# Performance work log

Hardware: AMD Instinct MI355X
Metric: run time of the kernel (lower is better)

The kernel has to match this reference:

```python
import jax, jax.numpy as jnp
import numpy as np

# dims per module source / chosen globals
B, LB = 4, 28            # new frames, buffered frames; M = B+LB = L = 32
DK, DV = 256, 32         # Dk=256 hardcoded; Dv = 4*len_of_lookup+4 with len_of_lookup=7
HS, WS = 64, 64          # H//8, W//8 with H=W=512
LMAX = 32                # memory cap L
TRAIN_SZ = 1000          # log base train_sz
ALPHA = 0.5              # blend coefficient (original inits 0, which zeroes the branch)
# log(L*h*w + h*w, train_sz) / sqrt(Dk)
SCALE = float(np.log(LMAX * HS * WS + HS * WS) / np.log(TRAIN_SZ) / np.sqrt(DK))


def _xavier(key, fan_in, fan_out):
    lim = np.sqrt(6.0 / (fan_in + fan_out))
    return jax.random.uniform(key, (fan_in, fan_out), jnp.float32, -lim, lim)


def setup_inputs() -> dict:
    key = jax.random.key(0)
    ks = jax.random.split(key, 7)
    return {
        "fc": jax.random.normal(ks[0], (B, DK, HS, WS), jnp.float32),
        "fm": jax.random.normal(ks[1], (B, DV, HS, WS), jnp.float32),
        "key_buffer": jax.random.normal(ks[2], (LB, DK, HS, WS), jnp.float32),
        "value_buffer": jax.random.normal(ks[3], (LB, DV, HS, WS), jnp.float32),
        "Q": _xavier(ks[4], DK, DK),
        "K": _xavier(ks[5], DK, DK),
        "V": _xavier(ks[6], DV, DV),
    }


def reference(fc, fm, key_buffer, value_buffer, Q, K, V):
    # matmul = einsum('ijkl,jm->imkl'): per-pixel channel mixing
    q = jnp.einsum('bdhw,de->behw', fc, Q)                      # [B,Dk,h,w]
    k = jnp.concatenate([jnp.einsum('bdhw,de->behw', fc, K), key_buffer], axis=0)    # [M,Dk,h,w]
    v = jnp.concatenate([jnp.einsum('bdhw,de->behw', fm, V), value_buffer], axis=0)  # [M,Dv,h,w]
    # current_batch (=1) < L, so no slicing of k/v on this step
    scores = SCALE * jnp.einsum('bdhw,mdhw->bmhw', q, k)        # [B,M,h,w]
    attn = jax.nn.softmax(scores, axis=-1)                      # NOTE: softmax over width axis, as in source (dim=-1)
    ctx = jnp.einsum('bmhw,mdhw->bdhw', attn, v)                # [B,Dv,h,w]
    return fm + ALPHA * ctx
```

## Files before the change

### kernel.cpp

```cpp
#include <hip/hip_runtime.h>
#include <hip/hip_bf16.h>
#include <cmath>

#define NB 4
#define NM 32
#define DKc 256
#define DVc 32
#define NP 4096

using bf16x8 = __attribute__((ext_vector_type(8))) short;
using f32x4  = __attribute__((ext_vector_type(4))) float;

__device__ __forceinline__ unsigned short f2bf(float f) {
    union { float f; unsigned u; } x; x.f = f;
    unsigned r = 0x7FFFu + ((x.u >> 16) & 1u);
    return (unsigned short)((x.u + r) >> 16);
}

__global__ __launch_bounds__(256) void k_prep(
    const float* __restrict__ fc, unsigned short* __restrict__ fcT,
    const float* __restrict__ Q, unsigned short* __restrict__ WTq,
    const float* __restrict__ K, unsigned short* __restrict__ WTk,
    const float* __restrict__ fm, const float* __restrict__ V, float* __restrict__ vproj) {
    int x = blockIdx.x;
    int t = threadIdx.x;
    if (x < 1056) {
        __shared__ float tile[64][65];
        const float* s; unsigned short* d; int R, C, r0, c0;
        if (x < 1024) {
            int bb = x >> 8, rest = x & 255;
            R = 256; C = 4096;
            r0 = (rest >> 6) * 64; c0 = (rest & 63) * 64;
            s = fc + (long)bb * 256 * 4096; d = fcT + (long)bb * 256 * 4096;
        } else {
            int i = x - 1024;
            int mat = i >> 4, idx = i & 15;
            R = 256; C = 256;
            r0 = (idx >> 2) * 64; c0 = (idx & 3) * 64;
            s = mat ? K : Q; d = mat ? WTk : WTq;
        }
        #pragma unroll
        for (int j = 0; j < 16; ++j) {
            int i = t + 256 * j;
            int r = i >> 6, c = i & 63;
            tile[r][c] = s[(long)(r0 + r) * C + c0 + c];
        }
        __syncthreads();
        #pragma unroll
        for (int j = 0; j < 8; ++j) {
            int i = t + 256 * j;
            int row = i >> 5;
            int pr = i & 31;
            float f0 = tile[2 * pr][row];
            float f1 = tile[2 * pr + 1][row];
            unsigned pack = (unsigned)f2bf(f0) | ((unsigned)f2bf(f1) << 16);
            reinterpret_cast<unsigned*>(d)[(((long)(c0 + row) * R + r0) >> 1) + pr] = pack;
        }
    } else {
        __shared__ float Vl[32][32];
        __shared__ float fml[32][256];
        int i = x - 1056;
        int b = i >> 4, p0 = (i & 15) * 256;
        #pragma unroll
        for (int j = 0; j < 4; ++j) { int ii = t + 256 * j; Vl[ii >> 5][ii & 31] = V[ii]; }
        for (int j = 0; j < 32; ++j) {
            int ii = t + 256 * j;
            int dd = ii >> 8, c = ii & 255;
            fml[dd][c] = fm[((long)b * DVc + dd) * NP + p0 + c];
        }
        __syncthreads();
        float acc[32];
        #pragma unroll
        for (int e = 0; e < 32; ++e) acc[e] = 0.f;
        for (int dd = 0; dd < 32; ++dd) {
            float fv = fml[dd][t];
            #pragma unroll
            for (int e = 0; e < 32; ++e) acc[e] += fv * Vl[dd][e];
        }
        #pragma unroll
        for (int e = 0; e < 32; ++e) vproj[((long)b * DVc + e) * NP + p0 + t] = acc[e];
    }
}

__global__ __launch_bounds__(256) void k_proj(
    const unsigned short* __restrict__ WTq, const unsigned short* __restrict__ WTk,
    const unsigned short* __restrict__ fcT,
    float* __restrict__ qproj, float* __restrict__ kproj) {
    int t = threadIdx.x;
    int wave = t >> 6, lane = t & 63;
    int y = blockIdx.y;
    int b = y & 3, mat = y >> 2;
    int p0 = blockIdx.x * 64;
    int ln = lane & 15, quad = lane >> 4;
    const unsigned short* WT = mat ? WTk : WTq;
    float* dst = mat ? kproj : qproj;
    int e0w = wave * 64;
    const unsigned short* bbase = fcT + ((long)b * NP + p0 + ln) * DKc + quad * 8;
    f32x4 acc[4][4] = {};
    for (int kk = 0; kk < DKc; kk += 32) {
        bf16x8 a[4], bb[4];
        #pragma unroll
        for (int i = 0; i < 4; ++i)
            a[i] = *reinterpret_cast<const bf16x8*>(WT + (long)(e0w + i * 16 + ln) * DKc + quad * 8 + kk);
        #pragma unroll
        for (int j = 0; j < 4; ++j)
            bb[j] = *reinterpret_cast<const bf16x8*>(bbase + (long)j * 16 * DKc + kk);
        #pragma unroll
        for (int i = 0; i < 4; ++i)
            #pragma unroll
            for (int j = 0; j < 4; ++j)
                acc[i][j] = __builtin_amdgcn_mfma_f32_16x16x32_bf16(a[i], bb[j], acc[i][j], 0, 0, 0);
    }
    #pragma unroll
    for (int i = 0; i < 4; ++i)
        #pragma unroll
        for (int j = 0; j < 4; ++j)
            #pragma unroll
            for (int r = 0; r < 4; ++r) {
                int e = e0w + i * 16 + quad * 4 + r, p = p0 + j * 16 + ln;
                dst[((long)b * DKc + e) * NP + p] = acc[i][j][r];
            }
}

__global__ __launch_bounds__(1024, 4) void k_fused(
    const float* __restrict__ qproj, const float* __restrict__ kproj,
    const float* __restrict__ kbuf, const float* __restrict__ vproj,
    const float* __restrict__ vbuf, const float* __restrict__ fm,
    float* __restrict__ out, float scale) {
    __shared__ float red[16 * 1099];
    __shared__ float sc[32][68];
    int t = threadIdx.x;
    int b = blockIdx.x >> 6, hrow = blockIdx.x & 63;
    int p0h = hrow * 64;
    int wave = t >> 6, lane = t & 63;
    int wq = lane & 15, egw = lane >> 4;
    int e0 = wave * 16 + egw * 4;
    int w0 = wq * 4;

    f32x4 qv[4];
    const float* qp = qproj + ((long)b * DKc + e0) * NP + p0h + w0;
    #pragma unroll
    for (int j = 0; j < 4; ++j) qv[j] = *reinterpret_cast<const f32x4*>(qp + (long)j * NP);

    #pragma unroll
    for (int mc = 0; mc < 2; ++mc) {
        f32x4 acc[16];
        #pragma unroll
        for (int mi = 0; mi < 16; ++mi) acc[mi] = (f32x4){0.f, 0.f, 0.f, 0.f};
        #pragma unroll
        for (int mi = 0; mi < 16; ++mi) {
            int m = mc * 16 + mi;
            const float* kp = (m < 4 ? kproj + (long)m * DKc * NP : kbuf + (long)(m - 4) * DKc * NP)
                              + (long)e0 * NP + p0h + w0;
            #pragma unroll
            for (int j = 0; j < 4; ++j) {
                f32x4 kv = *reinterpret_cast<const f32x4*>(kp + (long)j * NP);
                acc[mi] += qv[j] * kv;
            }
        }
        #pragma unroll
        for (int mi = 0; mi < 16; ++mi)
            #pragma unroll
            for (int c = 0; c < 4; ++c) {
                float v = acc[mi][c];
                v += __shfl_xor(v, 16);
                v += __shfl_xor(v, 32);
                acc[mi][c] = v;
            }
        if (lane < 16) {
            #pragma unroll
            for (int mi = 0; mi < 16; ++mi)
                *reinterpret_cast<f32x4*>(&red[wave * 1099 + mi * 69 + lane * 4]) = acc[mi];
        }
        __syncthreads();
        {
            int mr = t >> 6, w = t & 63;
            float s = 0.f;
            #pragma unroll
            for (int v = 0; v < 16; ++v) s += red[v * 1099 + mr * 69 + w];
            sc[mc * 16 + mr][w] = s * scale;
        }
        __syncthreads();
    }
    #pragma unroll
    for (int r = 0; r < 2; ++r) {
        int m = wave * 2 + r;
        float x = sc[m][lane];
        float mx = x;
        #pragma unroll
        for (int d = 1; d < 64; d <<= 1) mx = fmaxf(mx, __shfl_xor(mx, d));
        float e = __expf(x - mx);
        float sum = e;
        #pragma unroll
        for (int d = 1; d < 64; d <<= 1) sum += __shfl_xor(sum, d);
        sc[m][lane] = e / sum;
    }
    __syncthreads();
    {
        int dg = t >> 6, w = t & 63;
        float c0 = 0.f, c1 = 0.f;
        #pragma unroll
        for (int m = 0; m < NM; ++m) {
            float a = sc[m][w];
            const float* vp = (m < 4 ? vproj + (long)m * DVc * NP : vbuf + (long)(m - 4) * DVc * NP)
                              + (long)(dg * 2) * NP + p0h + w;
            c0 += a * vp[0];
            c1 += a * vp[NP];
        }
        long gi0 = ((long)b * DVc + dg * 2) * NP + p0h + w;
        long gi1 = gi0 + NP;
        out[gi0] = fm[gi0] + 0.5f * c0;
        out[gi1] = fm[gi1] + 0.5f * c1;
    }
}

extern "C" void kernel_launch(void* const* d_in, const int* in_sizes, int n_in,
                              void* d_out, int out_size, void* d_ws, size_t ws_size,
                              hipStream_t stream) {
    const float* fc = (const float*)d_in[0];
    const float* fm = (const float*)d_in[1];
    const float* kb = (const float*)d_in[2];
    const float* vb = (const float*)d_in[3];
    const float* Q  = (const float*)d_in[4];
    const float* K  = (const float*)d_in[5];
    const float* V  = (const float*)d_in[6];
    float* out = (float*)d_out;
    char* ws = (char*)d_ws;
    unsigned short* fcT   = (unsigned short*)(ws);
    unsigned short* WTq   = (unsigned short*)(ws + 8388608);
    unsigned short* WTk   = (unsigned short*)(ws + 8519680);
    float*          qproj = (float*)(ws + 8650752);
    float*          kproj = (float*)(ws + 25427968);
    float*          vproj = (float*)(ws + 42205184);
    float scale = (float)(log(135168.0) / log(1000.0) / 16.0);

    hipLaunchKernelGGL(k_prep, dim3(1120), dim3(256), 0, stream,
                       fc, fcT, Q, WTq, K, WTk, fm, V, vproj);
    hipLaunchKernelGGL(k_proj, dim3(64, 8), dim3(256), 0, stream,
                       WTq, WTk, fcT, qproj, kproj);
    hipLaunchKernelGGL(k_fused, dim3(256), dim3(1024), 0, stream,
                       qproj, kproj, kb, vproj, vb, fm, out, scale);
}
```

Measured before the change: 263.0 us.

## Split fused attention into score-partial kernel and softmax/output kernel

Replaces the single 1024-thread fused kernel with two kernels. k_scores computes partial q·k dot products over 32-channel chunks, using a grid spread over width segments, channel chunks and batch, with one pixel per thread and no LDS reduction. k_out sums the 8 partials, applies softmax and the value mix. The goal is more parallelism and simpler coalesced loads in the heavy key-read stage. The cost is an extra launch and a partial buffer round-trip through memory, and the partial buffer aliases the workspace region used by fcT.

```diff
diff --git a/kernel.cpp b/kernel.cpp
--- a/kernel.cpp
+++ b/kernel.cpp
@@ -122,69 +122,60 @@
             }
 }
 
-__global__ __launch_bounds__(1024, 4) void k_fused(
+__global__ __launch_bounds__(256, 2) void k_scores(
     const float* __restrict__ qproj, const float* __restrict__ kproj,
-    const float* __restrict__ kbuf, const float* __restrict__ vproj,
+    const float* __restrict__ kbuf, float* __restrict__ partial) {
+    int t = threadIdx.x;
+    int wseg = blockIdx.x, ec = blockIdx.y, b = blockIdx.z;
+    int w = wseg * 256 + t;
+    int e0 = ec * 32;
+    const float* qp = qproj + ((long)b * DKc + e0) * NP + w;
+    float acc[NM];
+    #pragma unroll
+    for (int m = 0; m < NM; ++m) acc[m] = 0.f;
+    #pragma unroll 2
+    for (int e = 0; e < 32; ++e) {
+        float qv = qp[(long)e * NP];
+        float kv[NM];
+        #pragma unroll
+        for (int m = 0; m < NM; ++m) {
+            const float* kp = (m < 4 ? kproj + (long)m * DKc * NP
+                                     : kbuf + (long)(m - 4) * DKc * NP);
+            kv[m] = kp[(long)(e0 + e) * NP + w];
+        }
+        #pragma unroll
+        for (int m = 0; m < NM; ++m) acc[m] += qv * kv[m];
+    }
+    float* pp = partial + (((long)b * 8 + ec) * NM) * NP + w;
+    #pragma unroll
+    for (int m = 0; m < NM; ++m) pp[(long)m * NP] = acc[m];
+}
+
+__global__ __launch_bounds__(512) void k_out(
+    const float* __restrict__ partial, const float* __restrict__ vproj,
     const float* __restrict__ vbuf, const float* __restrict__ fm,
     float* __restrict__ out, float scale) {
-    __shared__ float red[16 * 1099];
     __shared__ float sc[32][68];
     int t = threadIdx.x;
     int b = blockIdx.x >> 6, hrow = blockIdx.x & 63;
     int p0h = hrow * 64;
     int wave = t >> 6, lane = t & 63;
-    int wq = lane & 15, egw = lane >> 4;
-    int e0 = wave * 16 + egw * 4;
-    int w0 = wq * 4;
-
-    f32x4 qv[4];
-    const float* qp = qproj + ((long)b * DKc + e0) * NP + p0h + w0;
-    #pragma unroll
-    for (int j = 0; j < 4; ++j) qv[j] = *reinterpret_cast<const f32x4*>(qp + (long)j * NP);
-
-    #pragma unroll
-    for (int mc = 0; mc < 2; ++mc) {
-        f32x4 acc[16];
-        #pragma unroll
-        for (int mi = 0; mi < 16; ++mi) acc[mi] = (f32x4){0.f, 0.f, 0.f, 0.f};
-        #pragma unroll
-        for (int mi = 0; mi < 16; ++mi) {
-            int m = mc * 16 + mi;
-            const float* kp = (m < 4 ? kproj + (long)m * DKc * NP : kbuf + (long)(m - 4) * DKc * NP)
-                              + (long)e0 * NP + p0h + w0;
-            #pragma unroll
-            for (int j = 0; j < 4; ++j) {
-                f32x4 kv = *reinterpret_cast<const f32x4*>(kp + (long)j * NP);
-                acc[mi] += qv[j] * kv;
-            }
-        }
-        #pragma unroll
-        for (int mi = 0; mi < 16; ++mi)
-            #pragma unroll
-            for (int c = 0; c < 4; ++c) {
-                float v = acc[mi][c];
-                v += __shfl_xor(v, 16);
-                v += __shfl_xor(v, 32);
-                acc[mi][c] = v;
-            }
-        if (lane < 16) {
-            #pragma unroll
-            for (int mi = 0; mi < 16; ++mi)
-                *reinterpret_cast<f32x4*>(&red[wave * 1099 + mi * 69 + lane * 4]) = acc[mi];
-        }
-        __syncthreads();
-        {
-            int mr = t >> 6, w = t & 63;
-            float s = 0.f;
-            #pragma unroll
-            for (int v = 0; v < 16; ++v) s += red[v * 1099 + mr * 69 + w];
-            sc[mc * 16 + mr][w] = s * scale;
-        }
-        __syncthreads();
-    }
-    #pragma unroll
-    for (int r = 0; r < 2; ++r) {
-        int m = wave * 2 + r;
+    {
+        int w = t & 63, mg = t >> 6;
+        float s[4] = {0.f, 0.f, 0.f, 0.f};
+        #pragma unroll
+        for (int c = 0; c < 8; ++c) {
+            const float* pp = partial + (((long)b * 8 + c) * NM + mg * 4) * NP + p0h + w;
+            #pragma unroll
+            for (int mi = 0; mi < 4; ++mi) s[mi] += pp[(long)mi * NP];
+        }
+        #pragma unroll
+        for (int mi = 0; mi < 4; ++mi) sc[mg * 4 + mi][w] = s[mi] * scale;
+    }
+    __syncthreads();
+    #pragma unroll
+    for (int r = 0; r < 4; ++r) {
+        int m = wave * 4 + r;
         float x = sc[m][lane];
         float mx = x;
         #pragma unroll
@@ -198,19 +189,20 @@
     __syncthreads();
     {
         int dg = t >> 6, w = t & 63;
-        float c0 = 0.f, c1 = 0.f;
+        float c4[4] = {0.f, 0.f, 0.f, 0.f};
         #pragma unroll
         for (int m = 0; m < NM; ++m) {
             float a = sc[m][w];
             const float* vp = (m < 4 ? vproj + (long)m * DVc * NP : vbuf + (long)(m - 4) * DVc * NP)
-                              + (long)(dg * 2) * NP + p0h + w;
-            c0 += a * vp[0];
-            c1 += a * vp[NP];
-        }
-        long gi0 = ((long)b * DVc + dg * 2) * NP + p0h + w;
-        long gi1 = gi0 + NP;
-        out[gi0] = fm[gi0] + 0.5f * c0;
-        out[gi1] = fm[gi1] + 0.5f * c1;
+                              + (long)(dg * 4) * NP + p0h + w;
+            #pragma unroll
+            for (int i = 0; i < 4; ++i) c4[i] += a * vp[(long)i * NP];
+        }
+        #pragma unroll
+        for (int i = 0; i < 4; ++i) {
+            long gi = ((long)b * DVc + dg * 4 + i) * NP + p0h + w;
+            out[gi] = fm[gi] + 0.5f * c4[i];
+        }
     }
 }
 
@@ -226,18 +218,21 @@
     const float* V  = (const float*)d_in[6];
     float* out = (float*)d_out;
     char* ws = (char*)d_ws;
-    unsigned short* fcT   = (unsigned short*)(ws);
-    unsigned short* WTq   = (unsigned short*)(ws + 8388608);
-    unsigned short* WTk   = (unsigned short*)(ws + 8519680);
-    float*          qproj = (float*)(ws + 8650752);
-    float*          kproj = (float*)(ws + 25427968);
-    float*          vproj = (float*)(ws + 42205184);
+    float*          qproj = (float*)(ws);
+    float*          kproj = (float*)(ws + 16777216);
+    float*          vproj = (float*)(ws + 33554432);
+    unsigned short* fcT   = (unsigned short*)(ws + 35651584);
+    unsigned short* WTq   = (unsigned short*)(ws + 44040192);
+    unsigned short* WTk   = (unsigned short*)(ws + 44171264);
+    float*          partial = (float*)(ws + 35651584);
     float scale = (float)(log(135168.0) / log(1000.0) / 16.0);
 
     hipLaunchKernelGGL(k_prep, dim3(1120), dim3(256), 0, stream,
                        fc, fcT, Q, WTq, K, WTk, fm, V, vproj);
     hipLaunchKernelGGL(k_proj, dim3(64, 8), dim3(256), 0, stream,
                        WTq, WTk, fcT, qproj, kproj);
-    hipLaunchKernelGGL(k_fused, dim3(256), dim3(1024), 0, stream,
-                       qproj, kproj, kb, vproj, vb, fm, out, scale);
-}
+    hipLaunchKernelGGL(k_scores, dim3(16, 8, 4), dim3(256), 0, stream,
+                       qproj, kproj, kb, partial);
+    hipLaunchKernelGGL(k_out, dim3(256), dim3(512), 0, stream,
+                       partial, vproj, vb, fm, out, scale);
+}
```

Measured after the change: 266.9 us. No clear change (+1.5%).
